# Optimization experiments

Hardware: AMD Instinct MI355X
Metric: run time of the kernel (lower is better)

The kernel has to match this reference:

```python
import jax, jax.numpy as jnp
import numpy as np

B, S, F, H, T = 1024, 64, 2, 128, 24  # batch, src_len, n_features, hidden, output_length


def setup_inputs() -> dict:
    key = jax.random.key(0)
    ks = jax.random.split(key, 20)
    def p(k, shape):
        return jax.random.normal(k, shape, jnp.float32) * 0.05
    return {
        "x": jax.random.normal(ks[0], (B, S, F), jnp.float32),
        "prev_y": jnp.zeros((B, F), jnp.float32),
        # encoder 3-layer LSTM (PyTorch gate order i,f,g,o; b = b_ih + b_hh fused)
        "enc_Wih0": p(ks[1], (4 * H, F)),
        "enc_Whh0": p(ks[2], (4 * H, H)),
        "enc_b0": p(ks[3], (4 * H,)),
        "enc_Wih12": p(ks[4], (2, 4 * H, H)),
        "enc_Whh12": p(ks[5], (2, 4 * H, H)),
        "enc_b12": p(ks[6], (2, 4 * H)),
        # Bahdanau attention
        "attn_W": p(ks[7], (H, 2 * H)),
        "attn_b": p(ks[8], (H,)),
        "v_W": p(ks[9], (H,)),
        # decoder 3-layer LSTM, input size H+2
        "dec_Wih0": p(ks[10], (4 * H, H + 2)),
        "dec_Whh0": p(ks[11], (4 * H, H)),
        "dec_b0": p(ks[12], (4 * H,)),
        "dec_Wih12": p(ks[13], (2, 4 * H, H)),
        "dec_Whh12": p(ks[14], (2, 4 * H, H)),
        "dec_b12": p(ks[15], (2, 4 * H)),
        # output head Linear(2H, 2)
        "out_W": p(ks[16], (2, 2 * H)),
        "out_b": p(ks[17], (2,)),
    }


def _lstm_cell(xt, h, c, Wih, Whh, b):
    g = xt @ Wih.T + h @ Whh.T + b  # [B, 4H]
    i, f, gg, o = jnp.split(g, 4, axis=-1)
    c = jax.nn.sigmoid(f) * c + jax.nn.sigmoid(i) * jnp.tanh(gg)
    h = jax.nn.sigmoid(o) * jnp.tanh(c)
    return h, c


def _lstm_layer(xs, Wih, Whh, b):
    # xs: [S, B, in] -> hs [S, B, H], final (h, c)
    z = jnp.zeros((xs.shape[1], Whh.shape[1]), xs.dtype)
    def step(carry, xt):
        h, c = _lstm_cell(xt, carry[0], carry[1], Wih, Whh, b)
        return (h, c), h
    (hT, cT), hs = jax.lax.scan(step, (z, z), xs)
    return hs, hT, cT


def reference(x, prev_y, enc_Wih0, enc_Whh0, enc_b0, enc_Wih12, enc_Whh12, enc_b12,
              attn_W, attn_b, v_W, dec_Wih0, dec_Whh0, dec_b0, dec_Wih12, dec_Whh12,
              dec_b12, out_W, out_b):
    # ---- encoder: 3-layer LSTM over time ----
    hs, h0, c0 = _lstm_layer(jnp.swapaxes(x, 0, 1), enc_Wih0, enc_Whh0, enc_b0)
    hid, cel = [h0], [c0]
    for l in range(2):
        hs, hT, cT = _lstm_layer(hs, enc_Wih12[l], enc_Whh12[l], enc_b12[l])
        hid.append(hT); cel.append(cT)
    enc_out = jnp.swapaxes(hs, 0, 1)            # [B, S, H]
    h = jnp.stack(hid)                           # [3, B, H]
    c = jnp.stack(cel)

    def dec_step(carry, _):
        prev_out, h, c = carry
        h_top = h[2]                                             # top-layer hidden [B, H]
        a_in = jnp.concatenate(
            [jnp.broadcast_to(h_top[:, None, :], enc_out.shape), enc_out], axis=-1)  # [B, S, 2H]
        scores = jnp.tanh(a_in @ attn_W.T + attn_b) @ v_W        # [B, S]
        attw = jax.nn.softmax(scores, axis=1)
        weighted = jnp.einsum('bs,bsd->bd', attw, enc_out)        # [B, H]
        rnn_in = jnp.concatenate([prev_out, weighted], axis=-1)   # [B, H+2]
        h0n, c0n = _lstm_cell(rnn_in, h[0], c[0], dec_Wih0, dec_Whh0, dec_b0)
        h1n, c1n = _lstm_cell(h0n, h[1], c[1], dec_Wih12[0], dec_Whh12[0], dec_b12[0])
        h2n, c2n = _lstm_cell(h1n, h[2], c[2], dec_Wih12[1], dec_Whh12[1], dec_b12[1])
        out = jnp.concatenate([h2n, weighted], axis=-1) @ out_W.T + out_b  # [B, 2]
        return (out, jnp.stack([h0n, h1n, h2n]), jnp.stack([c0n, c1n, c2n])), out

    _, outs = jax.lax.scan(dec_step, (prev_y, h, c), None, length=T)
    return outs  # [T, B, 2]
```

## Files before the change

kernel.cpp:

```cpp
#include <hip/hip_runtime.h>
#include <hip/hip_fp16.h>

#define SEQ   64
#define HID   128
#define TOUT  24

typedef unsigned int u32;
typedef _Float16 f16;
typedef __attribute__((ext_vector_type(8))) f16 f16x8;
typedef __attribute__((ext_vector_type(4))) float f32x4;
#define MFMA __builtin_amdgcn_mfma_f32_16x16x32_f16

static __device__ __forceinline__ float sigm(float x){
  return __builtin_amdgcn_rcpf(1.f + __expf(-x));
}
static __device__ __forceinline__ float tanh_fast(float x){
  return fmaf(2.f, __builtin_amdgcn_rcpf(1.f + __expf(-2.f*x)), -1.f);
}

__global__ void prep_kernel(
    const float* __restrict__ eWih0,  const float* __restrict__ eWhh0,
    const float* __restrict__ eWih12, const float* __restrict__ eWhh12,
    const float* __restrict__ aW,
    const float* __restrict__ dWih0,  const float* __restrict__ dWhh0,
    const float* __restrict__ dWih12, const float* __restrict__ dWhh12,
    const float* __restrict__ oW,
    __half* __restrict__ wE0, __half* __restrict__ wE1, __half* __restrict__ wE2,
    __half* __restrict__ wD0, __half* __restrict__ wD1, __half* __restrict__ wD2,
    __half* __restrict__ wAh, __half* __restrict__ wAeF, float* __restrict__ wOT,
    float* __restrict__ dW2)
{
  int id = blockIdx.x*blockDim.x + threadIdx.x;
  if (id < 65536){
    int m=id, jj=m&7, l=(m>>3)&63, kt=(m>>9)&3, nt=m>>11;
    int col = nt*16 + (l&15), k = kt*32 + ((l>>4)<<3) + jj;
    wE0[m] = __float2half(eWhh0[col*128 + k]); return;
  }
  id -= 65536;
  if (id < 5*131072){
    int seg = id >> 17, m = id & 131071;
    int jj=m&7, l=(m>>3)&63, kt=(m>>9)&7, nt=m>>12;
    int col = nt*16 + (l&15), k = kt*32 + ((l>>4)<<3) + jj;
    float v;
    if (seg==0)      v = (k<128)? eWih12[col*128+k]         : eWhh12[col*128 + (k-128)];
    else if (seg==1) v = (k<128)? eWih12[65536+col*128+k]   : eWhh12[65536 + col*128 + (k-128)];
    else if (seg==2) v = (k<128)? dWih0[col*130 + 2 + k]    : dWhh0[col*128 + (k-128)];
    else if (seg==3) v = (k<128)? dWih12[col*128+k]         : dWhh12[col*128 + (k-128)];
    else             v = (k<128)? dWih12[65536+col*128+k]   : dWhh12[65536 + col*128 + (k-128)];
    __half* dst = (seg==0)?wE1:(seg==1)?wE2:(seg==2)?wD0:(seg==3)?wD1:wD2;
    dst[m] = __float2half(v); return;
  }
  id -= 5*131072;
  if (id < 16384){
    int m=id, jj=m&7, l=(m>>3)&63, kt=(m>>9)&3, nt=m>>11;
    int col = nt*16 + (l&15), k = kt*32 + ((l>>4)<<3) + jj;
    wAh[m] = __float2half(aW[col*256 + k]); return;
  }
  id -= 16384;
  if (id < 16384){
    int m=id, jj=m&7, l=(m>>3)&63, kt=(m>>9)&3, nt=m>>11;
    int col = nt*16 + (l&15), k = kt*32 + ((l>>4)<<3) + jj;
    wAeF[m] = __float2half(aW[col*256 + 128 + k]); return;
  }
  id -= 16384;
  if (id < 512){ int k=id>>1, jo=id&1; wOT[id] = oW[jo*256 + k]; return; }
  id -= 512;
  if (id < 1024){ int col=id>>1, ki=id&1; dW2[id] = dWih0[col*130 + ki]; return; }
}

__global__ __launch_bounds__(512) __attribute__((amdgpu_waves_per_eu(2, 2)))
void enc_kernel(
    const float* __restrict__ x, const float* __restrict__ eb0,
    const float* __restrict__ eb12, const float* __restrict__ eWih0,
    const __half* __restrict__ wE0, const __half* __restrict__ wE1,
    const __half* __restrict__ wE2,
    __half* __restrict__ hs0, __half* __restrict__ hs1,
    __half* __restrict__ carryH, float* __restrict__ carryC)
{
  __shared__ __align__(16) __half hT[2][2048];

  const int tid = threadIdx.x, w = tid>>6, lane = tid&63;
  const int l15 = lane&15, g4 = lane>>4;
  const int j = w*16 + l15;
  const int b16 = blockIdx.x*16;
  const int K0 = ((j>>5)*64 + ((j>>3)&3)*16)*8 + (j&7);

  __half* hs0b = hs0 + (size_t)blockIdx.x*131072;
  __half* hs1b = hs1 + (size_t)blockIdx.x*131072;

  for (int layer=0; layer<3; ++layer){
    const __half* W  = (layer==0)? wE0 : (layer==1)? wE1 : wE2;
    const float* bs  = (layer==0)? eb0 : (layer==1)? eb12 : (eb12+512);
    const __half* hinb  = (layer==1)? hs0b : hs1b;
    __half* houtb = (layer==0)? hs0b : (layer==1)? hs1b : nullptr;

    float bias[4];
#pragma unroll
    for (int g=0; g<4; ++g) bias[g] = bs[g*128 + j];
    float2 wx[4];
    if (layer==0){
#pragma unroll
      for (int g=0; g<4; ++g) wx[g] = *(const float2*)(eWih0 + (g*128+j)*2);
    }
    const f16x8* wb = (const f16x8*)W + lane;
    f16x8 Wh[16];
    if (layer==0){
#pragma unroll
      for (int g=0; g<4; ++g)
#pragma unroll
        for (int kt=0; kt<4; ++kt) Wh[g*4+kt] = wb[(size_t)((g*8+w)*4 + kt)*64];
    } else {
#pragma unroll
      for (int g=0; g<4; ++g)
#pragma unroll
        for (int kt=0; kt<4; ++kt) Wh[g*4+kt] = wb[(size_t)((g*8+w)*8 + 4 + kt)*64];
    }
    float c[4] = {0.f,0.f,0.f,0.f};
    ((u32*)hT[0])[tid] = 0u; ((u32*)hT[0])[tid+512] = 0u;
    __syncthreads();

    float2 xv[4]; f16x8 alo[4];
    if (layer==0){
#pragma unroll
      for (int q=0; q<4; ++q) xv[q] = *(const float2*)(x + ((size_t)(b16+g4*4+q)*SEQ + 0)*2);
    } else {
#pragma unroll
      for (int kt=0; kt<4; ++kt) alo[kt] = *(const f16x8*)(hinb + (kt*64+lane)*8);
    }

    int cur = 0;
    for (int t=0; t<SEQ; ++t){
      f16x8 wi[16];
      if (layer>0){
#pragma unroll
        for (int g=0; g<4; ++g)
#pragma unroll
          for (int kt=0; kt<4; ++kt) wi[g*4+kt] = wb[(size_t)((g*8+w)*8 + kt)*64];
      }
      f16x8 ah[4];
#pragma unroll
      for (int kt=0; kt<4; ++kt) ah[kt] = *(const f16x8*)(hT[cur] + (kt*64+lane)*8);
      float2 xcur[4]; f16x8 acur[4];
      if (layer==0){
#pragma unroll
        for (int q=0; q<4; ++q) xcur[q] = xv[q];
        if (t+1 < SEQ)
#pragma unroll
          for (int q=0; q<4; ++q) xv[q] = *(const float2*)(x + ((size_t)(b16+g4*4+q)*SEQ + t+1)*2);
      } else {
#pragma unroll
        for (int kt=0; kt<4; ++kt) acur[kt] = alo[kt];
        if (t+1 < SEQ)
#pragma unroll
          for (int kt=0; kt<4; ++kt) alo[kt] = *(const f16x8*)(hinb + (size_t)(t+1)*2048 + (kt*64+lane)*8);
      }
      f32x4 acc[4];
#pragma unroll
      for (int g=0; g<4; ++g) acc[g] = (f32x4){0.f,0.f,0.f,0.f};
#pragma unroll
      for (int g=0; g<4; ++g)
#pragma unroll
        for (int kt=0; kt<4; ++kt) acc[g] = MFMA(ah[kt], Wh[g*4+kt], acc[g], 0,0,0);
      if (layer>0){
#pragma unroll
        for (int g=0; g<4; ++g)
#pragma unroll
          for (int kt=0; kt<4; ++kt) acc[g] = MFMA(acur[kt], wi[g*4+kt], acc[g], 0,0,0);
      }
#pragma unroll
      for (int q=0; q<4; ++q){
        float gi = acc[0][q]+bias[0], gf = acc[1][q]+bias[1],
              gg = acc[2][q]+bias[2], go = acc[3][q]+bias[3];
        if (layer==0){
          gi += xcur[q].x*wx[0].x + xcur[q].y*wx[0].y;
          gf += xcur[q].x*wx[1].x + xcur[q].y*wx[1].y;
          gg += xcur[q].x*wx[2].x + xcur[q].y*wx[2].y;
          go += xcur[q].x*wx[3].x + xcur[q].y*wx[3].y;
        }
        float cn = fmaf(sigm(gf), c[q], sigm(gi)*tanh_fast(gg));
        float hn = sigm(go)*tanh_fast(cn);
        c[q] = cn;
        __half hh = __float2half(hn);
        hT[cur^1][K0 + (g4*4+q)*8] = hh;
        if (layer < 2){
          houtb[(size_t)t*2048 + K0 + (g4*4+q)*8] = hh;
        } else {
          int off = g4*32768 + q*8192 + (t>>4)*2048 + (j>>5)*512
                  + ((t&15) + ((j>>3)&3)*16)*8 + (j&7);
          hs0b[off] = hh;
        }
        if (t == SEQ-1){
          int ci = (layer*1024 + b16 + g4*4 + q)*128 + j;
          carryH[ci] = hh;
          carryC[ci] = cn;
        }
      }
      __syncthreads();
      cur ^= 1;
    }
    __syncthreads();
  }
}

#define LDQ(Q, g, kh) \
  Q[0] = wb[(size_t)((g)*64 + (kh)*4 + 0)*64]; \
  Q[1] = wb[(size_t)((g)*64 + (kh)*4 + 1)*64]; \
  Q[2] = wb[(size_t)((g)*64 + (kh)*4 + 2)*64]; \
  Q[3] = wb[(size_t)((g)*64 + (kh)*4 + 3)*64];
#define MM4(Q, A, g) \
  acc[g] = MFMA(A[0], Q[0], acc[g], 0,0,0); \
  acc[g] = MFMA(A[1], Q[1], acc[g], 0,0,0); \
  acc[g] = MFMA(A[2], Q[2], acc[g], 0,0,0); \
  acc[g] = MFMA(A[3], Q[3], acc[g], 0,0,0);

static __device__ __forceinline__ void dec_gemm(const __half* __restrict__ W,
    const __half* __restrict__ A0, const __half* __restrict__ A1,
    f32x4* acc, int lane, int w8)
{
  const f16x8* wb = (const f16x8*)W + (size_t)(w8*8)*64 + lane;
  f16x8 qA[4], qB[4], a0[4], a1[4];
  LDQ(qA, 0, 0)
  LDQ(qB, 1, 0)
#pragma unroll
  for (int kt=0; kt<4; ++kt) a0[kt] = *(const f16x8*)(A0 + (kt*64+lane)*8);
#pragma unroll
  for (int g=0; g<4; ++g) acc[g] = (f32x4){0.f,0.f,0.f,0.f};
  MM4(qA, a0, 0)  LDQ(qA, 2, 0)
  MM4(qB, a0, 1)  LDQ(qB, 3, 0)
#pragma unroll
  for (int kt=0; kt<4; ++kt) a1[kt] = *(const f16x8*)(A1 + (kt*64+lane)*8);
  MM4(qA, a0, 2)  LDQ(qA, 0, 1)
  MM4(qB, a0, 3)  LDQ(qB, 1, 1)
  MM4(qA, a1, 0)  LDQ(qA, 2, 1)
  MM4(qB, a1, 1)  LDQ(qB, 3, 1)
  MM4(qA, a1, 2)
  MM4(qB, a1, 3)
}

__global__ __launch_bounds__(512)
void dec_kernel(
    const float* __restrict__ prev_y, const float* __restrict__ db0,
    const float* __restrict__ db12, const float* __restrict__ ob,
    const float* __restrict__ ab, const float* __restrict__ vW,
    const __half* __restrict__ wD0, const __half* __restrict__ wD1,
    const __half* __restrict__ wD2, const __half* __restrict__ wAh,
    const __half* __restrict__ wAeF, const float* __restrict__ wOT,
    const float* __restrict__ dW2, const __half* __restrict__ encAg,
    const __half* __restrict__ carryH, const float* __restrict__ carryC,
    float* __restrict__ dout)
{
  __shared__ __align__(16) __half hT[4][2048];
  __shared__ float hp[4][132];
  __shared__ float scbF[256];
  __shared__ __align__(16) __half scb16h[256];
  __shared__ float po[4][2];
  __shared__ float vwl[128];
  extern __shared__ __align__(16) __half dyn[];
  __half* encBL = dyn;
  __half* epL   = dyn + 32768;

  const int tid = threadIdx.x, w = tid>>6, lane = tid&63;
  const int l15 = lane&15, g4 = lane>>4;
  const int d = blockIdx.x, b4 = d*4;
  const int w8 = (w + d) & 7;
  const int j = w8*16 + l15;
  const int K0 = ((j>>5)*64 + ((j>>3)&3)*16)*8 + (j&7);
  const __half* encAd = encAg + (size_t)(d>>2)*131072 + (size_t)(d&3)*32768;

  float cD[3][4];
  if (g4 == 0){
#pragma unroll
    for (int l=0; l<3; ++l)
#pragma unroll
      for (int q=0; q<4; ++q){
        int ci = (l*1024 + b4 + q)*128 + j;
        hT[1+l][K0 + q*8] = carryH[ci];
        cD[l][q] = carryC[ci];
      }
  }
  if (tid < 8) po[tid>>1][tid&1] = prev_y[(b4 + (tid>>1))*2 + (tid&1)];
  if (tid < 128) vwl[tid] = vW[tid];

#pragma unroll
  for (int it=0; it<8; ++it){
    int lin = it*512 + tid;
    f16x8 v = *(const f16x8*)(encAd + (size_t)lin*8);
    int laneA = lin&63, ktA = (lin>>6)&3, sb = (lin>>8)&3, r4 = (lin>>10)&3;
    int s  = sb*16 + (laneA&15);
    int d0 = ktA*32 + ((laneA>>4)<<3);
    int base = r4*8192 + ((d0>>4)*2 + (s>>5))*512 + (s&7);
    int lb0  = (d0&15) + ((s>>3)&3)*16;
    f16* eb = (f16*)encBL;
#pragma unroll
    for (int u=0; u<8; ++u) eb[base + (lb0+u)*8] = v[u];
  }
#pragma unroll
  for (int i=0; i<2; ++i){
    int mt = w*2 + i, r4 = mt>>2, sb = mt&3;
    f16x8 a[4];
#pragma unroll
    for (int kt=0; kt<4; ++kt)
      a[kt] = *(const f16x8*)(encAd + (size_t)(((r4*4+sb)*4 + kt)*64 + lane)*8);
    const f16x8* bw = (const f16x8*)wAeF + lane;
#pragma unroll
    for (int nt=0; nt<8; ++nt){
      int col = nt*16 + l15;
      float abv = ab[col];
      f32x4 acc = {abv, abv, abv, abv};
#pragma unroll
      for (int kt=0; kt<4; ++kt) acc = MFMA(a[kt], bw[(size_t)(nt*4+kt)*64], acc, 0,0,0);
      int srow = r4*64 + sb*16 + g4*4;
#pragma unroll
      for (int q=0; q<4; ++q) epL[(srow+q)*132 + col] = __float2half(acc[q]);
    }
  }
  __syncthreads();

  auto cell = [&](float* crl, const float* bdp, const float* dwp, __half* hdst,
                  const f32x4* acc){
    float b0 = bdp[j], b1 = bdp[128+j], b2 = bdp[256+j], b3 = bdp[384+j];
    float2 w0, w1, w2, w3;
    if (dwp){
      w0 = *(const float2*)(dwp + 2*j);
      w1 = *(const float2*)(dwp + 2*(128+j));
      w2 = *(const float2*)(dwp + 2*(256+j));
      w3 = *(const float2*)(dwp + 2*(384+j));
    }
#pragma unroll
    for (int q=0; q<4; ++q){
      float gi = acc[0][q]+b0, gf = acc[1][q]+b1, gg = acc[2][q]+b2, go = acc[3][q]+b3;
      if (dwp){
        float p0 = po[q][0], p1 = po[q][1];
        gi += p0*w0.x + p1*w0.y;
        gf += p0*w1.x + p1*w1.y;
        gg += p0*w2.x + p1*w2.y;
        go += p0*w3.x + p1*w3.y;
      }
      float cn = fmaf(sigm(gf), crl[q], sigm(gi)*tanh_fast(gg));
      float hn = sigm(go)*tanh_fast(cn);
      crl[q] = cn;
      hdst[K0 + q*8] = __float2half(hn);
    }
  };

  int zr = 0;
  for (int t=0; t<TOUT; ++t){
    asm volatile("" : "+v"(zr));
    const float*  db0t  = db0  + zr;
    const float*  db12t = db12 + zr;
    const float*  dW2t  = dW2  + zr;
    const __half* wAht  = wAh  + zr;

    {
      f16x8 a[4], wAhR[4];
      const f16x8* wbh = (const f16x8*)wAht + lane;
#pragma unroll
      for (int kt=0; kt<4; ++kt) wAhR[kt] = wbh[(size_t)(w8*4+kt)*64];
#pragma unroll
      for (int kt=0; kt<4; ++kt) a[kt] = *(const f16x8*)(hT[3] + (kt*64+lane)*8);
      f32x4 acc = {0.f,0.f,0.f,0.f};
#pragma unroll
      for (int kt=0; kt<4; ++kt) acc = MFMA(a[kt], wAhR[kt], acc, 0,0,0);
      if (g4 == 0){
#pragma unroll
        for (int q=0; q<4; ++q) hp[q][j] = acc[q];
      }
    }
    __syncthreads();
    {
      int rs = tid>>1, r = rs>>6, jh = tid&1;
      const __half* er = epL + rs*132 + jh*64;
      const float* hr = hp[r] + jh*64;
      const float* vr = vwl + jh*64;
      float sc = 0.f;
#pragma unroll
      for (int p=0; p<8; ++p){
        f16x8 e = *(const f16x8*)(er + p*8);
#pragma unroll
        for (int u=0; u<8; ++u)
          sc = fmaf(tanh_fast((float)e[u] + hr[p*8+u]), vr[p*8+u], sc);
      }
      sc += __shfl_xor(sc, 1);
      if (jh == 0) scbF[rs] = sc;
    }
    __syncthreads();
    if (tid < 256){
      float v = scbF[tid];
      float m = v;
#pragma unroll
      for (int off=32; off; off>>=1) m = fmaxf(m, __shfl_xor(m, off));
      float e = __expf(v - m);
      float sm = e;
#pragma unroll
      for (int off=32; off; off>>=1) sm += __shfl_xor(sm, off);
      scb16h[tid] = __float2half(e * __builtin_amdgcn_rcpf(sm));
    }
    __syncthreads();
    {
#pragma unroll
      for (int r=0; r<4; ++r){
        f32x4 acc = {0.f,0.f,0.f,0.f};
#pragma unroll
        for (int kt=0; kt<2; ++kt){
          f16x8 abc = *(const f16x8*)(scb16h + r*64 + kt*32 + g4*8);
          f16x8 b   = *(const f16x8*)(encBL + r*8192 + ((w8*2+kt)*64 + lane)*8);
          acc = MFMA(abc, b, acc, 0,0,0);
        }
        if (lane < 16) hT[0][K0 + r*8] = __float2half(acc[0]);
      }
    }
    __syncthreads();
    f32x4 acc[4];
    dec_gemm(wD0, hT[0], hT[1], acc, lane, w8);
    if (g4 == 0) cell(cD[0], db0t, dW2t, hT[1], acc);
    __syncthreads();
    dec_gemm(wD1, hT[1], hT[2], acc, lane, w8);
    if (g4 == 0) cell(cD[1], db12t, nullptr, hT[2], acc);
    __syncthreads();
    dec_gemm(wD2, hT[2], hT[3], acc, lane, w8);
    if (g4 == 0) cell(cD[2], db12t + 512, nullptr, hT[3], acc);
    __syncthreads();
    if (tid < 256){
      int r = tid>>6, kl = tid&63;
      int k2 = kl*2;
      int sl = ((k2>>5)*64 + r + ((k2>>3)&3)*16)*8 + (k2&7);
      float2 h2f = __half22float2(*(const __half2*)(hT[3] + sl));
      float2 wwf = __half22float2(*(const __half2*)(hT[0] + sl));
      float2 a0 = *(const float2*)(wOT + k2*2);
      float2 a1 = *(const float2*)(wOT + k2*2 + 2);
      float2 b0v = *(const float2*)(wOT + (128+k2)*2);
      float2 b1v = *(const float2*)(wOT + (128+k2)*2 + 2);
      float o0 = h2f.x*a0.x + h2f.y*a1.x + wwf.x*b0v.x + wwf.y*b1v.x;
      float o1 = h2f.x*a0.y + h2f.y*a1.y + wwf.x*b0v.y + wwf.y*b1v.y;
#pragma unroll
      for (int off=32; off; off>>=1){ o0 += __shfl_xor(o0, off); o1 += __shfl_xor(o1, off); }
      if (kl == 0){
        float v0 = o0 + ob[0], v1 = o1 + ob[1];
        size_t oi = ((size_t)t*1024 + b4 + r)*2;
        dout[oi] = v0; dout[oi+1] = v1;
        po[r][0] = v0; po[r][1] = v1;
      }
    }
  }
}

extern "C" void kernel_launch(void* const* d_in, const int* in_sizes, int n_in,
                              void* d_out, int out_size, void* d_ws, size_t ws_size,
                              hipStream_t stream) {
  const float* x      = (const float*)d_in[0];
  const float* prev_y = (const float*)d_in[1];
  const float* eWih0  = (const float*)d_in[2];
  const float* eWhh0  = (const float*)d_in[3];
  const float* eb0    = (const float*)d_in[4];
  const float* eWih12 = (const float*)d_in[5];
  const float* eWhh12 = (const float*)d_in[6];
  const float* eb12   = (const float*)d_in[7];
  const float* aW     = (const float*)d_in[8];
  const float* ab     = (const float*)d_in[9];
  const float* vW     = (const float*)d_in[10];
  const float* dWih0  = (const float*)d_in[11];
  const float* dWhh0  = (const float*)d_in[12];
  const float* db0    = (const float*)d_in[13];
  const float* dWih12 = (const float*)d_in[14];
  const float* dWhh12 = (const float*)d_in[15];
  const float* db12   = (const float*)d_in[16];
  const float* oW     = (const float*)d_in[17];
  const float* ob     = (const float*)d_in[18];

  __half* wE0  = (__half*)d_ws;
  __half* wE1  = wE0 + 65536;
  __half* wE2  = wE1 + 131072;
  __half* wD0  = wE2 + 131072;
  __half* wD1  = wD0 + 131072;
  __half* wD2  = wD1 + 131072;
  __half* wAh  = wD2 + 131072;
  __half* wAeF = wAh + 16384;
  float*  wOT  = (float*)(wAeF + 16384);
  float*  dW2  = wOT + 512;
  __half* hs0  = (__half*)(dW2 + 1024);
  __half* hs1  = hs0 + (size_t)64*131072;
  __half* carryH = hs1 + (size_t)64*131072;
  float*  carryC = (float*)(carryH + 393216);

  const int prepN = 65536 + 5*131072 + 16384 + 16384 + 512 + 1024;
  prep_kernel<<<(prepN + 255)/256, 256, 0, stream>>>(
      eWih0, eWhh0, eWih12, eWhh12, aW, dWih0, dWhh0, dWih12, dWhh12, oW,
      wE0, wE1, wE2, wD0, wD1, wD2, wAh, wAeF, wOT, dW2);

  enc_kernel<<<64, 512, 0, stream>>>(
      x, eb0, eb12, eWih0, wE0, wE1, wE2, hs0, hs1, carryH, carryC);

  const int dynB = (32768 + 256*132) * 2;
  hipFuncSetAttribute(reinterpret_cast<const void*>(dec_kernel),
                      hipFuncAttributeMaxDynamicSharedMemorySize, dynB);
  dec_kernel<<<256, 512, dynB, stream>>>(
      prev_y, db0, db12, ob, ab, vW, wD0, wD1, wD2, wAh, wAeF, wOT, dW2,
      hs0, carryH, carryC, (float*)d_out);
}
```

Before: 615.9 us.

## Process 8 batch rows per decoder block and read encoder B-operand from global

The decoder block now handles 8 batch rows instead of 4, halving the grid to 128 blocks so each block's per-step weight GEMMs serve twice as many rows. The encoder also writes the attention-weighted-sum operand in MFMA B layout to a new global buffer, so the decoder reads it from global/L2 rather than staging it in LDS. The score pass gives each thread one full row instead of splitting a row across two threads. This trades fewer blocks on a 256-CU part, and global-memory latency in the weighted-sum loop, for reuse of the decoder weight loads and a smaller LDS footprint.

```diff
diff --git a/kernel.cpp b/kernel.cpp
--- a/kernel.cpp
+++ b/kernel.cpp
@@ -74,7 +74,7 @@
     const float* __restrict__ eb12, const float* __restrict__ eWih0,
     const __half* __restrict__ wE0, const __half* __restrict__ wE1,
     const __half* __restrict__ wE2,
-    __half* __restrict__ hs0, __half* __restrict__ hs1,
+    __half* __restrict__ hs0, __half* __restrict__ hs1, __half* __restrict__ encBg,
     __half* __restrict__ carryH, float* __restrict__ carryC)
 {
   __shared__ __align__(16) __half hT[2][2048];
@@ -188,6 +188,8 @@
           int off = g4*32768 + q*8192 + (t>>4)*2048 + (j>>5)*512
                   + ((t&15) + ((j>>3)&3)*16)*8 + (j&7);
           hs0b[off] = hh;
+          int offB = (((j>>4)*2 + (t>>5))*64 + (j&15) + ((t>>3)&3)*16)*8 + (t&7);
+          encBg[(size_t)(b16 + g4*4 + q)*8192 + offB] = hh;
         }
         if (t == SEQ-1){
           int ci = (layer*1024 + b16 + g4*4 + q)*128 + j;
@@ -246,61 +248,53 @@
     const __half* __restrict__ wD2, const __half* __restrict__ wAh,
     const __half* __restrict__ wAeF, const float* __restrict__ wOT,
     const float* __restrict__ dW2, const __half* __restrict__ encAg,
+    const __half* __restrict__ encBg,
     const __half* __restrict__ carryH, const float* __restrict__ carryC,
     float* __restrict__ dout)
 {
   __shared__ __align__(16) __half hT[4][2048];
-  __shared__ float hp[4][132];
-  __shared__ float scbF[256];
-  __shared__ __align__(16) __half scb16h[256];
-  __shared__ float po[4][2];
+  __shared__ float hp[8][132];
+  __shared__ float scbF[512];
+  __shared__ __align__(16) __half scb16h[512];
+  __shared__ float po[8][2];
   __shared__ float vwl[128];
   extern __shared__ __align__(16) __half dyn[];
-  __half* encBL = dyn;
-  __half* epL   = dyn + 32768;
+  __half* epL = dyn;
 
   const int tid = threadIdx.x, w = tid>>6, lane = tid&63;
   const int l15 = lane&15, g4 = lane>>4;
-  const int d = blockIdx.x, b4 = d*4;
+  const int d = blockIdx.x, b8 = d*8;
   const int w8 = (w + d) & 7;
   const int j = w8*16 + l15;
   const int K0 = ((j>>5)*64 + ((j>>3)&3)*16)*8 + (j&7);
-  const __half* encAd = encAg + (size_t)(d>>2)*131072 + (size_t)(d&3)*32768;
+  const __half* encAd = encAg + (size_t)(d>>1)*131072 + (size_t)(d&1)*65536;
+  const __half* encBd = encBg + (size_t)b8*8192;
+
+#pragma unroll
+  for (int i=0; i<8; ++i) ((u32*)hT)[i*512 + tid] = 0u;
+  __syncthreads();
 
   float cD[3][4];
-  if (g4 == 0){
+  if (g4 < 2){
 #pragma unroll
     for (int l=0; l<3; ++l)
 #pragma unroll
       for (int q=0; q<4; ++q){
-        int ci = (l*1024 + b4 + q)*128 + j;
-        hT[1+l][K0 + q*8] = carryH[ci];
+        int ci = (l*1024 + b8 + g4*4 + q)*128 + j;
+        hT[1+l][K0 + (g4*4+q)*8] = carryH[ci];
         cD[l][q] = carryC[ci];
       }
   }
-  if (tid < 8) po[tid>>1][tid&1] = prev_y[(b4 + (tid>>1))*2 + (tid&1)];
+  if (tid < 16) po[tid>>1][tid&1] = prev_y[(b8 + (tid>>1))*2 + (tid&1)];
   if (tid < 128) vwl[tid] = vW[tid];
 
 #pragma unroll
-  for (int it=0; it<8; ++it){
-    int lin = it*512 + tid;
-    f16x8 v = *(const f16x8*)(encAd + (size_t)lin*8);
-    int laneA = lin&63, ktA = (lin>>6)&3, sb = (lin>>8)&3, r4 = (lin>>10)&3;
-    int s  = sb*16 + (laneA&15);
-    int d0 = ktA*32 + ((laneA>>4)<<3);
-    int base = r4*8192 + ((d0>>4)*2 + (s>>5))*512 + (s&7);
-    int lb0  = (d0&15) + ((s>>3)&3)*16;
-    f16* eb = (f16*)encBL;
-#pragma unroll
-    for (int u=0; u<8; ++u) eb[base + (lb0+u)*8] = v[u];
-  }
-#pragma unroll
-  for (int i=0; i<2; ++i){
-    int mt = w*2 + i, r4 = mt>>2, sb = mt&3;
+  for (int i=0; i<4; ++i){
+    int mt = w*4 + i, rq = mt>>2, sb = mt&3;
+    const __half* arow = encAd + (rq>>2)*32768 + ((rq&3)*4 + sb)*2048;
     f16x8 a[4];
 #pragma unroll
-    for (int kt=0; kt<4; ++kt)
-      a[kt] = *(const f16x8*)(encAd + (size_t)(((r4*4+sb)*4 + kt)*64 + lane)*8);
+    for (int kt=0; kt<4; ++kt) a[kt] = *(const f16x8*)(arow + (kt*64+lane)*8);
     const f16x8* bw = (const f16x8*)wAeF + lane;
 #pragma unroll
     for (int nt=0; nt<8; ++nt){
@@ -309,9 +303,9 @@
       f32x4 acc = {abv, abv, abv, abv};
 #pragma unroll
       for (int kt=0; kt<4; ++kt) acc = MFMA(a[kt], bw[(size_t)(nt*4+kt)*64], acc, 0,0,0);
-      int srow = r4*64 + sb*16 + g4*4;
-#pragma unroll
-      for (int q=0; q<4; ++q) epL[(srow+q)*132 + col] = __float2half(acc[q]);
+      int srow = rq*64 + sb*16 + g4*4;
+#pragma unroll
+      for (int q=0; q<4; ++q) epL[(srow+q)*130 + col] = __float2half(acc[q]);
     }
   }
   __syncthreads();
@@ -328,9 +322,10 @@
     }
 #pragma unroll
     for (int q=0; q<4; ++q){
+      int row = g4*4 + q;
       float gi = acc[0][q]+b0, gf = acc[1][q]+b1, gg = acc[2][q]+b2, go = acc[3][q]+b3;
       if (dwp){
-        float p0 = po[q][0], p1 = po[q][1];
+        float p0 = po[row][0], p1 = po[row][1];
         gi += p0*w0.x + p1*w0.y;
         gf += p0*w1.x + p1*w1.y;
         gg += p0*w2.x + p1*w2.y;
@@ -339,17 +334,17 @@
       float cn = fmaf(sigm(gf), crl[q], sigm(gi)*tanh_fast(gg));
       float hn = sigm(go)*tanh_fast(cn);
       crl[q] = cn;
-      hdst[K0 + q*8] = __float2half(hn);
+      hdst[K0 + row*8] = __float2half(hn);
     }
   };
 
   int zr = 0;
   for (int t=0; t<TOUT; ++t){
     asm volatile("" : "+v"(zr));
-    const float*  db0t  = db0  + zr;
+    const float*  db0t  = db0 + zr;
     const float*  db12t = db12 + zr;
-    const float*  dW2t  = dW2  + zr;
-    const __half* wAht  = wAh  + zr;
+    const float*  dW2t  = dW2 + zr;
+    const __half* wAht  = wAh + zr;
 
     {
       f16x8 a[4], wAhR[4];
@@ -361,30 +356,28 @@
       f32x4 acc = {0.f,0.f,0.f,0.f};
 #pragma unroll
       for (int kt=0; kt<4; ++kt) acc = MFMA(a[kt], wAhR[kt], acc, 0,0,0);
-      if (g4 == 0){
-#pragma unroll
-        for (int q=0; q<4; ++q) hp[q][j] = acc[q];
+      if (g4 < 2){
+#pragma unroll
+        for (int q=0; q<4; ++q) hp[g4*4+q][j] = acc[q];
       }
     }
     __syncthreads();
     {
-      int rs = tid>>1, r = rs>>6, jh = tid&1;
-      const __half* er = epL + rs*132 + jh*64;
-      const float* hr = hp[r] + jh*64;
-      const float* vr = vwl + jh*64;
+      int r = tid>>6;
+      const __half* er = epL + (size_t)tid*130;
+      const float* hr = hp[r];
       float sc = 0.f;
-#pragma unroll
-      for (int p=0; p<8; ++p){
+#pragma unroll 4
+      for (int p=0; p<16; ++p){
         f16x8 e = *(const f16x8*)(er + p*8);
 #pragma unroll
         for (int u=0; u<8; ++u)
-          sc = fmaf(tanh_fast((float)e[u] + hr[p*8+u]), vr[p*8+u], sc);
-      }
-      sc += __shfl_xor(sc, 1);
-      if (jh == 0) scbF[rs] = sc;
-    }
-    __syncthreads();
-    if (tid < 256){
+          sc = fmaf(tanh_fast((float)e[u] + hr[p*8+u]), vwl[p*8+u], sc);
+      }
+      scbF[tid] = sc;
+    }
+    __syncthreads();
+    {
       float v = scbF[tid];
       float m = v;
 #pragma unroll
@@ -398,12 +391,12 @@
     __syncthreads();
     {
 #pragma unroll
-      for (int r=0; r<4; ++r){
+      for (int r=0; r<8; ++r){
         f32x4 acc = {0.f,0.f,0.f,0.f};
 #pragma unroll
         for (int kt=0; kt<2; ++kt){
           f16x8 abc = *(const f16x8*)(scb16h + r*64 + kt*32 + g4*8);
-          f16x8 b   = *(const f16x8*)(encBL + r*8192 + ((w8*2+kt)*64 + lane)*8);
+          f16x8 b   = *(const f16x8*)(encBd + (size_t)r*8192 + ((w8*2+kt)*64 + lane)*8);
           acc = MFMA(abc, b, acc, 0,0,0);
         }
         if (lane < 16) hT[0][K0 + r*8] = __float2half(acc[0]);
@@ -412,18 +405,17 @@
     __syncthreads();
     f32x4 acc[4];
     dec_gemm(wD0, hT[0], hT[1], acc, lane, w8);
-    if (g4 == 0) cell(cD[0], db0t, dW2t, hT[1], acc);
+    if (g4 < 2) cell(cD[0], db0t, dW2t, hT[1], acc);
     __syncthreads();
     dec_gemm(wD1, hT[1], hT[2], acc, lane, w8);
-    if (g4 == 0) cell(cD[1], db12t, nullptr, hT[2], acc);
+    if (g4 < 2) cell(cD[1], db12t, nullptr, hT[2], acc);
     __syncthreads();
     dec_gemm(wD2, hT[2], hT[3], acc, lane, w8);
-    if (g4 == 0) cell(cD[2], db12t + 512, nullptr, hT[3], acc);
-    __syncthreads();
-    if (tid < 256){
-      int r = tid>>6, kl = tid&63;
-      int k2 = kl*2;
-      int sl = ((k2>>5)*64 + r + ((k2>>3)&3)*16)*8 + (k2&7);
+    if (g4 < 2) cell(cD[2], db12t + 512, nullptr, hT[3], acc);
+    __syncthreads();
+    {
+      int k2 = lane*2;
+      int sl = ((k2>>5)*64 + w + ((k2>>3)&3)*16)*8 + (k2&7);
       float2 h2f = __half22float2(*(const __half2*)(hT[3] + sl));
       float2 wwf = __half22float2(*(const __half2*)(hT[0] + sl));
       float2 a0 = *(const float2*)(wOT + k2*2);
@@ -434,11 +426,11 @@
       float o1 = h2f.x*a0.y + h2f.y*a1.y + wwf.x*b0v.y + wwf.y*b1v.y;
 #pragma unroll
       for (int off=32; off; off>>=1){ o0 += __shfl_xor(o0, off); o1 += __shfl_xor(o1, off); }
-      if (kl == 0){
+      if (lane == 0){
         float v0 = o0 + ob[0], v1 = o1 + ob[1];
-        size_t oi = ((size_t)t*1024 + b4 + r)*2;
+        size_t oi = ((size_t)t*1024 + b8 + w)*2;
         dout[oi] = v0; dout[oi+1] = v1;
-        po[r][0] = v0; po[r][1] = v1;
+        po[w][0] = v0; po[w][1] = v1;
       }
     }
   }
@@ -479,7 +471,8 @@
   float*  dW2  = wOT + 512;
   __half* hs0  = (__half*)(dW2 + 1024);
   __half* hs1  = hs0 + (size_t)64*131072;
-  __half* carryH = hs1 + (size_t)64*131072;
+  __half* encB = hs1 + (size_t)64*131072;
+  __half* carryH = encB + (size_t)1024*8192;
   float*  carryC = (float*)(carryH + 393216);
 
   const int prepN = 65536 + 5*131072 + 16384 + 16384 + 512 + 1024;
@@ -488,12 +481,12 @@
       wE0, wE1, wE2, wD0, wD1, wD2, wAh, wAeF, wOT, dW2);
 
   enc_kernel<<<64, 512, 0, stream>>>(
-      x, eb0, eb12, eWih0, wE0, wE1, wE2, hs0, hs1, carryH, carryC);
-
-  const int dynB = (32768 + 256*132) * 2;
+      x, eb0, eb12, eWih0, wE0, wE1, wE2, hs0, hs1, encB, carryH, carryC);
+
+  const int dynB = 512*130*2;
   hipFuncSetAttribute(reinterpret_cast<const void*>(dec_kernel),
                       hipFuncAttributeMaxDynamicSharedMemorySize, dynB);
-  dec_kernel<<<256, 512, dynB, stream>>>(
+  dec_kernel<<<128, 512, dynB, stream>>>(
       prev_y, db0, db12, ob, ab, vW, wD0, wD1, wD2, wAh, wAeF, wOT, dW2,
-      hs0, carryH, carryC, (float*)d_out);
-}
+      hs0, encB, carryH, carryC, (float*)d_out);
+}
```

Result: slower. 990.1 us (+60.8%).

## Batch encoder input projections over 8-step chunks and use nontemporal decoder weight loads

Applied to the files above, without the earlier changes.

In encoder layers 1 and 2, the input-to-hidden projection for 8 timesteps is now computed in a batch ahead of the recurrence. The input weights are loaded once per chunk instead of every step, and the gate pre-activations are stored to a per-block global scratch buffer in fp16. The recurrent loop then reads these back as accumulator seeds, which removes the input MFMAs and weight reloads from the serial critical path. It adds global write/read traffic and rounds the input contribution to fp16. Decoder weight loads are also marked nontemporal, to reduce cache pollution.

```diff
diff --git a/kernel.cpp b/kernel.cpp
--- a/kernel.cpp
+++ b/kernel.cpp
@@ -74,7 +74,7 @@
     const float* __restrict__ eb12, const float* __restrict__ eWih0,
     const __half* __restrict__ wE0, const __half* __restrict__ wE1,
     const __half* __restrict__ wE2,
-    __half* __restrict__ hs0, __half* __restrict__ hs1,
+    __half* __restrict__ hs0, __half* __restrict__ hs1, __half2* __restrict__ ginB,
     __half* __restrict__ carryH, float* __restrict__ carryC)
 {
   __shared__ __align__(16) __half hT[2][2048];
@@ -87,6 +87,7 @@
 
   __half* hs0b = hs0 + (size_t)blockIdx.x*131072;
   __half* hs1b = hs1 + (size_t)blockIdx.x*131072;
+  __half2* GB  = ginB + (size_t)blockIdx.x*32768;
 
   for (int layer=0; layer<3; ++layer){
     const __half* W  = (layer==0)? wE0 : (layer==1)? wE1 : wE2;
@@ -119,94 +120,108 @@
     ((u32*)hT[0])[tid] = 0u; ((u32*)hT[0])[tid+512] = 0u;
     __syncthreads();
 
-    float2 xv[4]; f16x8 alo[4];
+    float2 xv[4];
     if (layer==0){
 #pragma unroll
       for (int q=0; q<4; ++q) xv[q] = *(const float2*)(x + ((size_t)(b16+g4*4+q)*SEQ + 0)*2);
-    } else {
-#pragma unroll
-      for (int kt=0; kt<4; ++kt) alo[kt] = *(const f16x8*)(hinb + (kt*64+lane)*8);
     }
 
     int cur = 0;
-    for (int t=0; t<SEQ; ++t){
-      f16x8 wi[16];
+    for (int tb=0; tb<SEQ; tb+=8){
       if (layer>0){
+        f16x8 Wi[16];
 #pragma unroll
         for (int g=0; g<4; ++g)
 #pragma unroll
-          for (int kt=0; kt<4; ++kt) wi[g*4+kt] = wb[(size_t)((g*8+w)*8 + kt)*64];
-      }
-      f16x8 ah[4];
-#pragma unroll
-      for (int kt=0; kt<4; ++kt) ah[kt] = *(const f16x8*)(hT[cur] + (kt*64+lane)*8);
-      float2 xcur[4]; f16x8 acur[4];
-      if (layer==0){
-#pragma unroll
-        for (int q=0; q<4; ++q) xcur[q] = xv[q];
-        if (t+1 < SEQ)
-#pragma unroll
-          for (int q=0; q<4; ++q) xv[q] = *(const float2*)(x + ((size_t)(b16+g4*4+q)*SEQ + t+1)*2);
-      } else {
-#pragma unroll
-        for (int kt=0; kt<4; ++kt) acur[kt] = alo[kt];
-        if (t+1 < SEQ)
-#pragma unroll
-          for (int kt=0; kt<4; ++kt) alo[kt] = *(const f16x8*)(hinb + (size_t)(t+1)*2048 + (kt*64+lane)*8);
-      }
-      f32x4 acc[4];
-#pragma unroll
-      for (int g=0; g<4; ++g) acc[g] = (f32x4){0.f,0.f,0.f,0.f};
-#pragma unroll
-      for (int g=0; g<4; ++g)
-#pragma unroll
-        for (int kt=0; kt<4; ++kt) acc[g] = MFMA(ah[kt], Wh[g*4+kt], acc[g], 0,0,0);
-      if (layer>0){
+          for (int kt=0; kt<4; ++kt) Wi[g*4+kt] = wb[(size_t)((g*8+w)*8 + kt)*64];
+        for (int tl=0; tl<8; ++tl){
+          int t = tb+tl;
+          f16x8 a2[4];
+#pragma unroll
+          for (int kt=0; kt<4; ++kt)
+            a2[kt] = *(const f16x8*)(hinb + (size_t)t*2048 + (kt*64+lane)*8);
+#pragma unroll
+          for (int g=0; g<4; ++g){
+            f32x4 acc = {0.f,0.f,0.f,0.f};
+#pragma unroll
+            for (int kt=0; kt<4; ++kt) acc = MFMA(a2[kt], Wi[g*4+kt], acc, 0,0,0);
+            __half2* gp = GB + ((((tl*8 + w)*4 + g)*64 + lane)*2);
+            gp[0] = __floats2half2_rn(acc[0], acc[1]);
+            gp[1] = __floats2half2_rn(acc[2], acc[3]);
+          }
+        }
+      }
+      for (int tl=0; tl<8; ++tl){
+        int t = tb+tl;
+        f32x4 acc[4];
+        if (layer>0){
+#pragma unroll
+          for (int g=0; g<4; ++g){
+            const __half2* gp = GB + ((((tl*8 + w)*4 + g)*64 + lane)*2);
+            float2 lo = __half22float2(gp[0]);
+            float2 hi = __half22float2(gp[1]);
+            acc[g] = (f32x4){lo.x, lo.y, hi.x, hi.y};
+          }
+        } else {
+#pragma unroll
+          for (int g=0; g<4; ++g) acc[g] = (f32x4){0.f,0.f,0.f,0.f};
+        }
+        f16x8 ah[4];
+#pragma unroll
+        for (int kt=0; kt<4; ++kt) ah[kt] = *(const f16x8*)(hT[cur] + (kt*64+lane)*8);
+        float2 xcur[4];
+        if (layer==0){
+#pragma unroll
+          for (int q=0; q<4; ++q) xcur[q] = xv[q];
+          if (t+1 < SEQ)
+#pragma unroll
+            for (int q=0; q<4; ++q) xv[q] = *(const float2*)(x + ((size_t)(b16+g4*4+q)*SEQ + t+1)*2);
+        }
 #pragma unroll
         for (int g=0; g<4; ++g)
 #pragma unroll
-          for (int kt=0; kt<4; ++kt) acc[g] = MFMA(acur[kt], wi[g*4+kt], acc[g], 0,0,0);
-      }
-#pragma unroll
-      for (int q=0; q<4; ++q){
-        float gi = acc[0][q]+bias[0], gf = acc[1][q]+bias[1],
-              gg = acc[2][q]+bias[2], go = acc[3][q]+bias[3];
-        if (layer==0){
-          gi += xcur[q].x*wx[0].x + xcur[q].y*wx[0].y;
-          gf += xcur[q].x*wx[1].x + xcur[q].y*wx[1].y;
-          gg += xcur[q].x*wx[2].x + xcur[q].y*wx[2].y;
-          go += xcur[q].x*wx[3].x + xcur[q].y*wx[3].y;
+          for (int kt=0; kt<4; ++kt) acc[g] = MFMA(ah[kt], Wh[g*4+kt], acc[g], 0,0,0);
+#pragma unroll
+        for (int q=0; q<4; ++q){
+          float gi = acc[0][q]+bias[0], gf = acc[1][q]+bias[1],
+                gg = acc[2][q]+bias[2], go = acc[3][q]+bias[3];
+          if (layer==0){
+            gi += xcur[q].x*wx[0].x + xcur[q].y*wx[0].y;
+            gf += xcur[q].x*wx[1].x + xcur[q].y*wx[1].y;
+            gg += xcur[q].x*wx[2].x + xcur[q].y*wx[2].y;
+            go += xcur[q].x*wx[3].x + xcur[q].y*wx[3].y;
+          }
+          float cn = fmaf(sigm(gf), c[q], sigm(gi)*tanh_fast(gg));
+          float hn = sigm(go)*tanh_fast(cn);
+          c[q] = cn;
+          __half hh = __float2half(hn);
+          hT[cur^1][K0 + (g4*4+q)*8] = hh;
+          if (layer < 2){
+            houtb[(size_t)t*2048 + K0 + (g4*4+q)*8] = hh;
+          } else {
+            int off = g4*32768 + q*8192 + (t>>4)*2048 + (j>>5)*512
+                    + ((t&15) + ((j>>3)&3)*16)*8 + (j&7);
+            hs0b[off] = hh;
+          }
+          if (t == SEQ-1){
+            int ci = (layer*1024 + b16 + g4*4 + q)*128 + j;
+            carryH[ci] = hh;
+            carryC[ci] = cn;
+          }
         }
-        float cn = fmaf(sigm(gf), c[q], sigm(gi)*tanh_fast(gg));
-        float hn = sigm(go)*tanh_fast(cn);
-        c[q] = cn;
-        __half hh = __float2half(hn);
-        hT[cur^1][K0 + (g4*4+q)*8] = hh;
-        if (layer < 2){
-          houtb[(size_t)t*2048 + K0 + (g4*4+q)*8] = hh;
-        } else {
-          int off = g4*32768 + q*8192 + (t>>4)*2048 + (j>>5)*512
-                  + ((t&15) + ((j>>3)&3)*16)*8 + (j&7);
-          hs0b[off] = hh;
-        }
-        if (t == SEQ-1){
-          int ci = (layer*1024 + b16 + g4*4 + q)*128 + j;
-          carryH[ci] = hh;
-          carryC[ci] = cn;
-        }
-      }
-      __syncthreads();
-      cur ^= 1;
+        __syncthreads();
+        cur ^= 1;
+      }
     }
     __syncthreads();
   }
 }
 
 #define LDQ(Q, g, kh) \
-  Q[0] = wb[(size_t)((g)*64 + (kh)*4 + 0)*64]; \
-  Q[1] = wb[(size_t)((g)*64 + (kh)*4 + 1)*64]; \
-  Q[2] = wb[(size_t)((g)*64 + (kh)*4 + 2)*64]; \
-  Q[3] = wb[(size_t)((g)*64 + (kh)*4 + 3)*64];
+  Q[0] = __builtin_nontemporal_load(&wb[(size_t)((g)*64 + (kh)*4 + 0)*64]); \
+  Q[1] = __builtin_nontemporal_load(&wb[(size_t)((g)*64 + (kh)*4 + 1)*64]); \
+  Q[2] = __builtin_nontemporal_load(&wb[(size_t)((g)*64 + (kh)*4 + 2)*64]); \
+  Q[3] = __builtin_nontemporal_load(&wb[(size_t)((g)*64 + (kh)*4 + 3)*64]);
 #define MM4(Q, A, g) \
   acc[g] = MFMA(A[0], Q[0], acc[g], 0,0,0); \
   acc[g] = MFMA(A[1], Q[1], acc[g], 0,0,0); \
@@ -355,7 +370,8 @@
       f16x8 a[4], wAhR[4];
       const f16x8* wbh = (const f16x8*)wAht + lane;
 #pragma unroll
-      for (int kt=0; kt<4; ++kt) wAhR[kt] = wbh[(size_t)(w8*4+kt)*64];
+      for (int kt=0; kt<4; ++kt)
+        wAhR[kt] = __builtin_nontemporal_load(&wbh[(size_t)(w8*4+kt)*64]);
 #pragma unroll
       for (int kt=0; kt<4; ++kt) a[kt] = *(const f16x8*)(hT[3] + (kt*64+lane)*8);
       f32x4 acc = {0.f,0.f,0.f,0.f};
@@ -481,6 +497,7 @@
   __half* hs1  = hs0 + (size_t)64*131072;
   __half* carryH = hs1 + (size_t)64*131072;
   float*  carryC = (float*)(carryH + 393216);
+  __half2* ginB  = (__half2*)(carryC + 393216);
 
   const int prepN = 65536 + 5*131072 + 16384 + 16384 + 512 + 1024;
   prep_kernel<<<(prepN + 255)/256, 256, 0, stream>>>(
@@ -488,7 +505,7 @@
       wE0, wE1, wE2, wD0, wD1, wD2, wAh, wAeF, wOT, dW2);
 
   enc_kernel<<<64, 512, 0, stream>>>(
-      x, eb0, eb12, eWih0, wE0, wE1, wE2, hs0, hs1, carryH, carryC);
+      x, eb0, eb12, eWih0, wE0, wE1, wE2, hs0, hs1, ginB, carryH, carryC);
 
   const int dynB = (32768 + 256*132) * 2;
   hipFuncSetAttribute(reinterpret_cast<const void*>(dec_kernel),
```

After: 1.214 ms. 97.2% more time.
